# Kernel optimization log

Hardware: AMD Instinct MI355X
Metric: run time of the kernel (lower is better)

The kernel has to match this reference:

```python
import jax, jax.numpy as jnp
import numpy as np

B, DIM, HEADS, H, W = 4, 192, 6, 256, 256
C = DIM // HEADS  # channels per head
DN = ('NCHW', 'OIHW', 'NCHW')


def conv2d(x, w, b, padding='VALID', groups=1):
    y = jax.lax.conv_general_dilated(x, w, (1, 1), padding,
                                     dimension_numbers=DN,
                                     feature_group_count=groups)
    return y + b[None, :, None, None]


def setup_inputs() -> dict:
    key = jax.random.key(0)
    ks = jax.random.split(key, 8)
    s = 0.02
    return {
        'x': jax.random.normal(ks[0], (B, DIM, H, W), jnp.float32),
        'qkv_w': jax.random.normal(ks[1], (3 * DIM, DIM, 1, 1), jnp.float32) * s,
        'qkv_b': jnp.zeros((3 * DIM,), jnp.float32),
        'dw_w': jax.random.normal(ks[2], (3 * DIM, 1, 3, 3), jnp.float32) * s,
        'dw_b': jnp.zeros((3 * DIM,), jnp.float32),
        'proj_w': jax.random.normal(ks[3], (DIM, DIM, 1, 1), jnp.float32) * s,
        'proj_b': jnp.zeros((DIM,), jnp.float32),
        'temperature': jnp.ones((HEADS, 1, 1, 1), jnp.float32),
    }


def reference(x, qkv_w, qkv_b, dw_w, dw_b, proj_w, proj_b, temperature):
    # qkv projection: 1x1 conv then 3x3 depthwise conv
    qkv = conv2d(x, qkv_w, qkv_b)
    qkv = conv2d(qkv, dw_w, dw_b, padding='SAME', groups=3 * DIM)
    q, k, v = jnp.split(qkv, 3, axis=1)  # each (B, DIM, H, W)

    def heads(t):
        return t.reshape(B, HEADS, C, H, W)
    q, k, v = heads(q), heads(k), heads(v)

    # L2-normalize along W (matches F.normalize eps=1e-12)
    eps = 1e-12
    q = q / jnp.maximum(jnp.linalg.norm(q, axis=-1, keepdims=True), eps)
    k = k / jnp.maximum(jnp.linalg.norm(k, axis=-1, keepdims=True), eps)

    # per-channel HxH attention, contraction over W; temperature broadcasts over head
    attn = jnp.einsum('bncxw,bncyw->bncxy', q, k) * temperature  # (B,HEADS,C,H,H)
    attn = jax.nn.softmax(attn, axis=-1)
    out = jnp.einsum('bncxy,bncyw->bncxw', attn, v)  # (B,HEADS,C,H,W)

    out = out.reshape(B, DIM, H, W)
    return conv2d(out, proj_w, proj_b)
```

## Files before the change

### kernel.cpp

```cpp
#include <hip/hip_runtime.h>
#include <hip/hip_bf16.h>
#include <math.h>


#define HW 65536
#define IMW 256

typedef short bf16x8 __attribute__((ext_vector_type(8)));
typedef float f32x4  __attribute__((ext_vector_type(4)));

__device__ __forceinline__ float bf2f(ushort u) {
    return __uint_as_float((uint)u << 16);
}
__device__ __forceinline__ ushort f2bf(float f) {
    uint i = __float_as_uint(f);
    return (ushort)((i + 0x7FFFu + ((i >> 16) & 1u)) >> 16);
}

__device__ __forceinline__ void gload16(const ushort* g, ushort* l) {
    __builtin_amdgcn_global_load_lds(
        (const __attribute__((address_space(1))) void*)g,
        (__attribute__((address_space(3))) void*)l,
        16, 0, 0);
}

__global__ __launch_bounds__(256) void cvt_f32_bf16(const float* __restrict__ s,
                                                    ushort* __restrict__ d, int n)
{
    int i = blockIdx.x * 256 + threadIdx.x;
    if (i < n) d[i] = f2bf(s[i]);
}

__global__ __launch_bounds__(256) void cvt_transpose_f32(const float* __restrict__ src,
                                                         ushort* __restrict__ dst,
                                                         int R, int C,
                                                         long ssS, long ssD)
{
    __shared__ ushort Ls[64][72];
    int t = threadIdx.x;
    long z = blockIdx.z;
    src += z * ssS; dst += z * ssD;
    int c0 = blockIdx.x * 64, r0 = blockIdx.y * 64;
    {
        int r = t >> 2, cs = t & 3;
        const float* gp = src + (size_t)(r0 + r) * C + c0 + cs * 16;
        ushort tmp[16];
        #pragma unroll
        for (int q = 0; q < 4; ++q) {
            float4 v = *(const float4*)(gp + q * 4);
            tmp[q*4+0] = f2bf(v.x); tmp[q*4+1] = f2bf(v.y);
            tmp[q*4+2] = f2bf(v.z); tmp[q*4+3] = f2bf(v.w);
        }
        *(uint4*)&Ls[r][cs * 16]     = *(uint4*)&tmp[0];
        *(uint4*)&Ls[r][cs * 16 + 8] = *(uint4*)&tmp[8];
    }
    __syncthreads();
    {
        int cc = t & 63, seg = t >> 6;
        ushort tmp[16];
        #pragma unroll
        for (int j = 0; j < 16; ++j) tmp[j] = Ls[seg * 16 + j][cc];
        ushort* op = dst + (size_t)(c0 + cc) * R + r0 + seg * 16;
        *(uint4*)(op)     = *(uint4*)&tmp[0];
        *(uint4*)(op + 8) = *(uint4*)&tmp[8];
    }
}

__global__ __launch_bounds__(256) void transpose_bf16(const ushort* __restrict__ src,
                                                      ushort* __restrict__ dst,
                                                      int R, int C,
                                                      long ssS, long ssD)
{
    __shared__ ushort Ls[64][72];
    int t = threadIdx.x;
    long z = blockIdx.z;
    src += z * ssS; dst += z * ssD;
    int c0 = blockIdx.x * 64, r0 = blockIdx.y * 64;
    {
        int r = t >> 2, cs = t & 3;
        const ushort* gp = src + (size_t)(r0 + r) * C + c0 + cs * 16;
        *(uint4*)&Ls[r][cs * 16]     = *(const uint4*)(gp);
        *(uint4*)&Ls[r][cs * 16 + 8] = *(const uint4*)(gp + 8);
    }
    __syncthreads();
    {
        int cc = t & 63, seg = t >> 6;
        ushort tmp[16];
        #pragma unroll
        for (int j = 0; j < 16; ++j) tmp[j] = Ls[seg * 16 + j][cc];
        ushort* op = dst + (size_t)(c0 + cc) * R + r0 + seg * 16;
        *(uint4*)(op)     = *(uint4*)&tmp[0];
        *(uint4*)(op + 8) = *(uint4*)&tmp[8];
    }
}

__global__ __launch_bounds__(256) void transpose_v(const ushort* __restrict__ post,
                                                   ushort* __restrict__ vt)
{
    __shared__ ushort Ls[64][72];
    int t = threadIdx.x;
    int s = blockIdx.z;
    int b = s / 192, r = s - b * 192;
    const ushort* src = post + ((size_t)b * 576 + 384 + r) * HW;
    ushort*       dst = vt + (size_t)s * HW;
    int c0 = blockIdx.x * 64, r0 = blockIdx.y * 64;
    {
        int rr = t >> 2, cs = t & 3;
        const ushort* gp = src + (size_t)(r0 + rr) * IMW + c0 + cs * 16;
        *(uint4*)&Ls[rr][cs * 16]     = *(const uint4*)(gp);
        *(uint4*)&Ls[rr][cs * 16 + 8] = *(const uint4*)(gp + 8);
    }
    __syncthreads();
    {
        int cc = t & 63, seg = t >> 6;
        ushort tmp[16];
        #pragma unroll
        for (int j = 0; j < 16; ++j) tmp[j] = Ls[seg * 16 + j][cc];
        ushort* op = dst + (size_t)(c0 + cc) * IMW + r0 + seg * 16;
        *(uint4*)(op)     = *(uint4*)&tmp[0];
        *(uint4*)(op + 8) = *(uint4*)&tmp[8];
    }
}

__global__ __launch_bounds__(256) void gemm_mfma(const ushort* __restrict__ A, int lda, long sliceA,
                                                 const ushort* __restrict__ B, int ldb, long sliceB,
                                                 void* __restrict__ Dp, int ldd, long sliceD,
                                                 const float* __restrict__ bias,
                                                 int K, int outF32, int NM, int NN)
{
    int lin = blockIdx.x;
    int r8 = lin & 7, kk_ = lin >> 3;
    int m = kk_ % NM, fg = kk_ / NM;
    int g = fg * 8 + r8;
    int nt_ = g % NN;
    long z = g / NN;
    int m0 = m * 64;
    int n0 = nt_ * 256;

    __shared__ ushort Ws[2][64][32];
    __shared__ ushort Xs[2][256][32];
    int t = threadIdx.x, wv = t >> 6, lane = t & 63;
    int fr = lane & 15, sg = lane >> 4;
    A += z * sliceA; B += z * sliceB;

    int rl   = wv * 16 + (lane >> 2);
    int chnk = (lane & 3) ^ ((lane >> 3) & 3);
    const ushort* srcA  = A + (size_t)(m0 + rl) * lda + chnk * 8;
    const ushort* srcB0 = B + (size_t)(n0 +       rl) * ldb + chnk * 8;
    const ushort* srcB1 = B + (size_t)(n0 +  64 + rl) * ldb + chnk * 8;
    const ushort* srcB2 = B + (size_t)(n0 + 128 + rl) * ldb + chnk * 8;
    const ushort* srcB3 = B + (size_t)(n0 + 192 + rl) * ldb + chnk * 8;

    int sp = sg ^ ((fr >> 1) & 3);

    f32x4 acc[4][4];
    #pragma unroll
    for (int i = 0; i < 4; ++i)
        #pragma unroll
        for (int j = 0; j < 4; ++j) acc[i][j] = (f32x4){0.f, 0.f, 0.f, 0.f};

    gload16(srcA,  &Ws[0][wv * 16][0]);
    gload16(srcB0, &Xs[0][      wv * 16][0]);
    gload16(srcB1, &Xs[0][ 64 + wv * 16][0]);
    gload16(srcB2, &Xs[0][128 + wv * 16][0]);
    gload16(srcB3, &Xs[0][192 + wv * 16][0]);
    __syncthreads();

    int nkit = K >> 5;
    for (int kit = 0; kit < nkit; ++kit) {
        int cur = kit & 1;
        if (kit + 1 < nkit) {
            int kn = (kit + 1) * 32;
            gload16(srcA  + kn, &Ws[cur ^ 1][wv * 16][0]);
            gload16(srcB0 + kn, &Xs[cur ^ 1][      wv * 16][0]);
            gload16(srcB1 + kn, &Xs[cur ^ 1][ 64 + wv * 16][0]);
            gload16(srcB2 + kn, &Xs[cur ^ 1][128 + wv * 16][0]);
            gload16(srcB3 + kn, &Xs[cur ^ 1][192 + wv * 16][0]);
        }
        bf16x8 a[4];
        #pragma unroll
        for (int i = 0; i < 4; ++i)
            a[i] = *(const bf16x8*)&Ws[cur][i * 16 + fr][sp * 8];
        #pragma unroll
        for (int j = 0; j < 4; ++j) {
            bf16x8 b = *(const bf16x8*)&Xs[cur][wv * 64 + j * 16 + fr][sp * 8];
            #pragma unroll
            for (int i = 0; i < 4; ++i)
                acc[i][j] = __builtin_amdgcn_mfma_f32_16x16x32_bf16(a[i], b, acc[i][j], 0, 0, 0);
        }
        __syncthreads();
    }

    int nw0 = n0 + wv * 64;
    int rbase = sg * 4;
    if (outF32) {
        float* D = (float*)Dp + z * sliceD;
        #pragma unroll
        for (int i = 0; i < 4; ++i) {
            #pragma unroll
            for (int r_ = 0; r_ < 4; ++r_) {
                int mrow = m0 + i * 16 + rbase + r_;
                float bv = bias ? bias[mrow] : 0.f;
                #pragma unroll
                for (int j = 0; j < 4; ++j)
                    D[(size_t)mrow * ldd + nw0 + j * 16 + fr] = acc[i][j][r_] + bv;
            }
        }
    } else {
        ushort* D = (ushort*)Dp + z * sliceD;
        #pragma unroll
        for (int i = 0; i < 4; ++i) {
            #pragma unroll
            for (int r_ = 0; r_ < 4; ++r_) {
                int mrow = m0 + i * 16 + rbase + r_;
                float bv = bias ? bias[mrow] : 0.f;
                #pragma unroll
                for (int j = 0; j < 4; ++j)
                    D[(size_t)mrow * ldd + nw0 + j * 16 + fr] = f2bf(acc[i][j][r_] + bv);
            }
        }
    }
}

__global__ __launch_bounds__(256) void attn_fused(const ushort* __restrict__ post,
                                                  const ushort* __restrict__ vt,
                                                  const float* __restrict__ temp,
                                                  ushort* __restrict__ O)
{
    __shared__ ushort Ws[64][32];
    __shared__ ushort Xs[256][32];
    __shared__ ushort Ps[64][264];
    int t = threadIdx.x, wv = t >> 6, lane = t & 63;
    int fr = lane & 15, sg = lane >> 4;
    int lin = blockIdx.x;
    int r8 = lin & 7, k_ = lin >> 3;
    int mtile = k_ & 3, fg = k_ >> 2;
    int s = fg * 8 + r8;
    int b = s / 192, ch = s - b * 192;
    const ushort* Aq = post + ((size_t)b * 576 + ch) * HW;
    const ushort* Bk = Aq + (size_t)192 * HW;
    const ushort* Vt = vt + (size_t)s * HW;
    int m0 = mtile * 64;

    int rl   = wv * 16 + (lane >> 2);
    int chnk = (lane & 3) ^ ((lane >> 3) & 3);
    int sp   = sg ^ ((fr >> 1) & 3);
    const ushort* srcQ  = Aq + (size_t)(m0 + rl) * IMW + chnk * 8;
    const ushort* srcK0 = Bk + (size_t)(      rl) * IMW + chnk * 8;
    const ushort* srcK1 = Bk + (size_t)( 64 + rl) * IMW + chnk * 8;
    const ushort* srcK2 = Bk + (size_t)(128 + rl) * IMW + chnk * 8;
    const ushort* srcK3 = Bk + (size_t)(192 + rl) * IMW + chnk * 8;
    const ushort* srcV0 = Vt + (size_t)(      rl) * IMW + chnk * 8;
    const ushort* srcV1 = Vt + (size_t)( 64 + rl) * IMW + chnk * 8;
    const ushort* srcV2 = Vt + (size_t)(128 + rl) * IMW + chnk * 8;
    const ushort* srcV3 = Vt + (size_t)(192 + rl) * IMW + chnk * 8;

    f32x4 acc[16];
    #pragma unroll
    for (int i = 0; i < 16; ++i) acc[i] = (f32x4){0.f, 0.f, 0.f, 0.f};

    for (int k0 = 0; k0 < 256; k0 += 32) {
        gload16(srcQ  + k0, &Ws[wv * 16][0]);
        gload16(srcK0 + k0, &Xs[      wv * 16][0]);
        gload16(srcK1 + k0, &Xs[ 64 + wv * 16][0]);
        gload16(srcK2 + k0, &Xs[128 + wv * 16][0]);
        gload16(srcK3 + k0, &Xs[192 + wv * 16][0]);
        __syncthreads();
        bf16x8 a = *(const bf16x8*)&Ws[wv * 16 + fr][sp * 8];
        #pragma unroll
        for (int nt = 0; nt < 16; ++nt) {
            bf16x8 bfrag = *(const bf16x8*)&Xs[nt * 16 + fr][sp * 8];
            acc[nt] = __builtin_amdgcn_mfma_f32_16x16x32_bf16(a, bfrag, acc[nt], 0, 0, 0);
        }
        __syncthreads();
    }

    float tv = temp[ch >> 5];
    #pragma unroll
    for (int r_ = 0; r_ < 4; ++r_) {
        float v[16];
        float mx = -3.4e38f;
        #pragma unroll
        for (int nt = 0; nt < 16; ++nt) { v[nt] = acc[nt][r_] * tv; mx = fmaxf(mx, v[nt]); }
        #pragma unroll
        for (int sh = 1; sh < 16; sh <<= 1) mx = fmaxf(mx, __shfl_xor(mx, sh, 64));
        float sum = 0.f;
        #pragma unroll
        for (int nt = 0; nt < 16; ++nt) { v[nt] = __expf(v[nt] - mx); sum += v[nt]; }
        #pragma unroll
        for (int sh = 1; sh < 16; sh <<= 1) sum += __shfl_xor(sum, sh, 64);
        float inv = 1.f / sum;
        int ml = wv * 16 + sg * 4 + r_;
        #pragma unroll
        for (int nt = 0; nt < 16; ++nt)
            Ps[ml][fr + nt * 16] = f2bf(v[nt] * inv);
    }

    f32x4 acc2[16];
    #pragma unroll
    for (int i = 0; i < 16; ++i) acc2[i] = (f32x4){0.f, 0.f, 0.f, 0.f};

    for (int y0 = 0; y0 < 256; y0 += 32) {
        gload16(srcV0 + y0, &Xs[      wv * 16][0]);
        gload16(srcV1 + y0, &Xs[ 64 + wv * 16][0]);
        gload16(srcV2 + y0, &Xs[128 + wv * 16][0]);
        gload16(srcV3 + y0, &Xs[192 + wv * 16][0]);
        __syncthreads();
        bf16x8 a = *(const bf16x8*)&Ps[wv * 16 + fr][y0 + sg * 8];
        #pragma unroll
        for (int nt = 0; nt < 16; ++nt) {
            bf16x8 bfrag = *(const bf16x8*)&Xs[nt * 16 + fr][sp * 8];
            acc2[nt] = __builtin_amdgcn_mfma_f32_16x16x32_bf16(a, bfrag, acc2[nt], 0, 0, 0);
        }
        __syncthreads();
    }

    ushort* Op = O + (size_t)s * HW;
    int mrow = m0 + wv * 16 + sg * 4;
    #pragma unroll
    for (int r_ = 0; r_ < 4; ++r_) {
        #pragma unroll
        for (int nt = 0; nt < 16; ++nt)
            Op[(size_t)(mrow + r_) * IMW + fr + nt * 16] = f2bf(acc2[nt][r_]);
    }
}

__global__ __launch_bounds__(256) void dw3x3_l2norm(const ushort* __restrict__ in,
                                                    const float* __restrict__ w,
                                                    const float* __restrict__ bias,
                                                    ushort* __restrict__ out)
{
    int t = threadIdx.x;
    int lane = t & 63, wv = t >> 6;
    int ch = blockIdx.y;
    int r0 = blockIdx.x * 16 + wv * 4;
    const ushort* img  = in  + ((size_t)blockIdx.z * 576 + ch) * HW;
    ushort*       outp = out + ((size_t)blockIdx.z * 576 + ch) * HW;
    int px = lane * 4;

    float rv[6][4], lv[6], rx[6];
    #pragma unroll
    for (int i = 0; i < 6; ++i) {
        int rr = r0 - 1 + i;
        if ((unsigned)rr <= 255u) {
            ushort4 cv = *(const ushort4*)&img[(size_t)rr * IMW + px];
            rv[i][0] = bf2f(cv.x); rv[i][1] = bf2f(cv.y);
            rv[i][2] = bf2f(cv.z); rv[i][3] = bf2f(cv.w);
        } else {
            rv[i][0] = rv[i][1] = rv[i][2] = rv[i][3] = 0.f;
        }
        float l = __shfl_up(rv[i][3], 1, 64);
        lv[i] = (lane == 0) ? 0.f : l;
        float r = __shfl_down(rv[i][0], 1, 64);
        rx[i] = (lane == 63) ? 0.f : r;
    }

    const float* wch = w + ch * 9;
    float bv = bias[ch];
    bool do_norm = (ch < 384);

    #pragma unroll
    for (int j = 0; j < 4; ++j) {
        float a0 = bv, a1 = bv, a2 = bv, a3 = bv;
        #pragma unroll
        for (int dy = 0; dy < 3; ++dy) {
            int i = j + dy;
            float w0 = wch[dy * 3], w1 = wch[dy * 3 + 1], w2 = wch[dy * 3 + 2];
            a0 += lv[i]    * w0 + rv[i][0] * w1 + rv[i][1] * w2;
            a1 += rv[i][0] * w0 + rv[i][1] * w1 + rv[i][2] * w2;
            a2 += rv[i][1] * w0 + rv[i][2] * w1 + rv[i][3] * w2;
            a3 += rv[i][2] * w0 + rv[i][3] * w1 + rx[i]    * w2;
        }
        if (do_norm) {
            float ss = a0 * a0 + a1 * a1 + a2 * a2 + a3 * a3;
            #pragma unroll
            for (int m = 1; m < 64; m <<= 1) ss += __shfl_xor(ss, m, 64);
            float inv = 1.0f / fmaxf(sqrtf(ss), 1e-12f);
            a0 *= inv; a1 *= inv; a2 *= inv; a3 *= inv;
        }
        ushort4 o;
        o.x = f2bf(a0); o.y = f2bf(a1); o.z = f2bf(a2); o.w = f2bf(a3);
        *(ushort4*)&outp[(size_t)(r0 + j) * IMW + px] = o;
    }
}

extern "C" void kernel_launch(void* const* d_in, const int* in_sizes, int n_in,
                              void* d_out, int out_size, void* d_ws, size_t ws_size,
                              hipStream_t stream)
{
    const float* x      = (const float*)d_in[0];
    const float* qkv_w  = (const float*)d_in[1];
    const float* qkv_b  = (const float*)d_in[2];
    const float* dw_w   = (const float*)d_in[3];
    const float* dw_b   = (const float*)d_in[4];
    const float* proj_w = (const float*)d_in[5];
    const float* proj_b = (const float*)d_in[6];
    const float* temp   = (const float*)d_in[7];
    float* out = (float*)d_out;

    const size_t off_wq   = 0;
    const size_t off_wp   = 110592;
    const size_t off_pre  = 262144;
    const size_t off_post = off_pre + (size_t)4 * 576 * HW;
    const size_t off_xt   = off_post + (size_t)4 * 576 * HW;
    const size_t total_us = off_xt + (size_t)4 * 192 * HW;
    if (ws_size < total_us * sizeof(ushort)) return;

    ushort* wsb  = (ushort*)d_ws;
    ushort* wq   = wsb + off_wq;
    ushort* wp   = wsb + off_wp;
    ushort* pre  = wsb + off_pre;
    ushort* post = wsb + off_post;
    ushort* xt   = wsb + off_xt;
    ushort* Obuf = pre;
    ushort* Otb  = pre + (size_t)4 * 192 * HW;

    const long SL = (long)192 * HW;

    cvt_f32_bf16<<<dim3(432), 256, 0, stream>>>(qkv_w, wq, 110592);
    cvt_f32_bf16<<<dim3(144), 256, 0, stream>>>(proj_w, wp, 36864);

    cvt_transpose_f32<<<dim3(1024, 3, 4), 256, 0, stream>>>(x, xt, 192, HW, SL, SL);
    gemm_mfma<<<dim3(9 * 256 * 4), 256, 0, stream>>>(wq, 192, 0, xt, 192, SL,
                                                     pre, HW, (long)576 * HW,
                                                     qkv_b, 192, 0, 9, 256);
    dw3x3_l2norm<<<dim3(16, 576, 4), 256, 0, stream>>>(pre, dw_w, dw_b, post);
    transpose_v<<<dim3(4, 4, 768), 256, 0, stream>>>(post, xt);
    attn_fused<<<dim3(4 * 768), 256, 0, stream>>>(post, xt, temp, Obuf);
    transpose_bf16<<<dim3(1024, 3, 4), 256, 0, stream>>>(Obuf, Otb, 192, HW, SL, SL);
    gemm_mfma<<<dim3(3 * 256 * 4), 256, 0, stream>>>(wp, 192, 0, Otb, 192, SL,
                                                     out, HW, SL,
                                                     proj_b, 192, 1, 3, 256);
}
```

Measured before the change: 687.7 us.

## Double-buffer LDS loads in fused attention and enlarge depthwise row tiles

Both GEMM phases of the fused attention kernel now use two LDS buffers, so the global-to-LDS load of the next K chunk is issued before computing the current one, and one barrier per iteration is dropped. The first V tile is prefetched while the softmax runs. Separately, the depthwise 3x3 plus L2-norm kernel now has each wave process 8 rows instead of 4, which cuts the halo reloads by half and launches half as many blocks. LDS use for the K/V staging doubles and the depthwise kernel holds more registers, which may reduce occupancy.

Result: slower. 718.5 us (+4.5%).

```diff
diff --git a/kernel.cpp b/kernel.cpp
--- a/kernel.cpp
+++ b/kernel.cpp
@@ -227,8 +227,8 @@
                                                   const float* __restrict__ temp,
                                                   ushort* __restrict__ O)
 {
-    __shared__ ushort Ws[64][32];
-    __shared__ ushort Xs[256][32];
+    __shared__ ushort Ws[2][64][32];
+    __shared__ ushort Xs[2][256][32];
     __shared__ ushort Ps[64][264];
     int t = threadIdx.x, wv = t >> 6, lane = t & 63;
     int fr = lane & 15, sg = lane >> 4;
@@ -259,21 +259,36 @@
     #pragma unroll
     for (int i = 0; i < 16; ++i) acc[i] = (f32x4){0.f, 0.f, 0.f, 0.f};
 
-    for (int k0 = 0; k0 < 256; k0 += 32) {
-        gload16(srcQ  + k0, &Ws[wv * 16][0]);
-        gload16(srcK0 + k0, &Xs[      wv * 16][0]);
-        gload16(srcK1 + k0, &Xs[ 64 + wv * 16][0]);
-        gload16(srcK2 + k0, &Xs[128 + wv * 16][0]);
-        gload16(srcK3 + k0, &Xs[192 + wv * 16][0]);
+    gload16(srcQ,  &Ws[0][wv * 16][0]);
+    gload16(srcK0, &Xs[0][      wv * 16][0]);
+    gload16(srcK1, &Xs[0][ 64 + wv * 16][0]);
+    gload16(srcK2, &Xs[0][128 + wv * 16][0]);
+    gload16(srcK3, &Xs[0][192 + wv * 16][0]);
+    __syncthreads();
+
+    for (int kit = 0; kit < 8; ++kit) {
+        int cur = kit & 1;
+        if (kit < 7) {
+            int kn = (kit + 1) * 32;
+            gload16(srcQ  + kn, &Ws[cur ^ 1][wv * 16][0]);
+            gload16(srcK0 + kn, &Xs[cur ^ 1][      wv * 16][0]);
+            gload16(srcK1 + kn, &Xs[cur ^ 1][ 64 + wv * 16][0]);
+            gload16(srcK2 + kn, &Xs[cur ^ 1][128 + wv * 16][0]);
+            gload16(srcK3 + kn, &Xs[cur ^ 1][192 + wv * 16][0]);
+        }
+        bf16x8 a = *(const bf16x8*)&Ws[cur][wv * 16 + fr][sp * 8];
+        #pragma unroll
+        for (int nt = 0; nt < 16; ++nt) {
+            bf16x8 bfrag = *(const bf16x8*)&Xs[cur][nt * 16 + fr][sp * 8];
+            acc[nt] = __builtin_amdgcn_mfma_f32_16x16x32_bf16(a, bfrag, acc[nt], 0, 0, 0);
+        }
         __syncthreads();
-        bf16x8 a = *(const bf16x8*)&Ws[wv * 16 + fr][sp * 8];
-        #pragma unroll
-        for (int nt = 0; nt < 16; ++nt) {
-            bf16x8 bfrag = *(const bf16x8*)&Xs[nt * 16 + fr][sp * 8];
-            acc[nt] = __builtin_amdgcn_mfma_f32_16x16x32_bf16(a, bfrag, acc[nt], 0, 0, 0);
-        }
-        __syncthreads();
-    }
+    }
+
+    gload16(srcV0, &Xs[0][      wv * 16][0]);
+    gload16(srcV1, &Xs[0][ 64 + wv * 16][0]);
+    gload16(srcV2, &Xs[0][128 + wv * 16][0]);
+    gload16(srcV3, &Xs[0][192 + wv * 16][0]);
 
     float tv = temp[ch >> 5];
     #pragma unroll
@@ -295,21 +310,25 @@
         for (int nt = 0; nt < 16; ++nt)
             Ps[ml][fr + nt * 16] = f2bf(v[nt] * inv);
     }
+    __syncthreads();
 
     f32x4 acc2[16];
     #pragma unroll
     for (int i = 0; i < 16; ++i) acc2[i] = (f32x4){0.f, 0.f, 0.f, 0.f};
 
-    for (int y0 = 0; y0 < 256; y0 += 32) {
-        gload16(srcV0 + y0, &Xs[      wv * 16][0]);
-        gload16(srcV1 + y0, &Xs[ 64 + wv * 16][0]);
-        gload16(srcV2 + y0, &Xs[128 + wv * 16][0]);
-        gload16(srcV3 + y0, &Xs[192 + wv * 16][0]);
-        __syncthreads();
-        bf16x8 a = *(const bf16x8*)&Ps[wv * 16 + fr][y0 + sg * 8];
+    for (int y = 0; y < 8; ++y) {
+        int cur = y & 1;
+        if (y < 7) {
+            int yn = (y + 1) * 32;
+            gload16(srcV0 + yn, &Xs[cur ^ 1][      wv * 16][0]);
+            gload16(srcV1 + yn, &Xs[cur ^ 1][ 64 + wv * 16][0]);
+            gload16(srcV2 + yn, &Xs[cur ^ 1][128 + wv * 16][0]);
+            gload16(srcV3 + yn, &Xs[cur ^ 1][192 + wv * 16][0]);
+        }
+        bf16x8 a = *(const bf16x8*)&Ps[wv * 16 + fr][y * 32 + sg * 8];
         #pragma unroll
         for (int nt = 0; nt < 16; ++nt) {
-            bf16x8 bfrag = *(const bf16x8*)&Xs[nt * 16 + fr][sp * 8];
+            bf16x8 bfrag = *(const bf16x8*)&Xs[cur][nt * 16 + fr][sp * 8];
             acc2[nt] = __builtin_amdgcn_mfma_f32_16x16x32_bf16(a, bfrag, acc2[nt], 0, 0, 0);
         }
         __syncthreads();
@@ -333,14 +352,14 @@
     int t = threadIdx.x;
     int lane = t & 63, wv = t >> 6;
     int ch = blockIdx.y;
-    int r0 = blockIdx.x * 16 + wv * 4;
+    int r0 = blockIdx.x * 32 + wv * 8;
     const ushort* img  = in  + ((size_t)blockIdx.z * 576 + ch) * HW;
     ushort*       outp = out + ((size_t)blockIdx.z * 576 + ch) * HW;
     int px = lane * 4;
 
-    float rv[6][4], lv[6], rx[6];
-    #pragma unroll
-    for (int i = 0; i < 6; ++i) {
+    float rv[10][4], lv[10], rx[10];
+    #pragma unroll
+    for (int i = 0; i < 10; ++i) {
         int rr = r0 - 1 + i;
         if ((unsigned)rr <= 255u) {
             ushort4 cv = *(const ushort4*)&img[(size_t)rr * IMW + px];
@@ -360,7 +379,7 @@
     bool do_norm = (ch < 384);
 
     #pragma unroll
-    for (int j = 0; j < 4; ++j) {
+    for (int j = 0; j < 8; ++j) {
         float a0 = bv, a1 = bv, a2 = bv, a3 = bv;
         #pragma unroll
         for (int dy = 0; dy < 3; ++dy) {
@@ -424,7 +443,7 @@
     gemm_mfma<<<dim3(9 * 256 * 4), 256, 0, stream>>>(wq, 192, 0, xt, 192, SL,
                                                      pre, HW, (long)576 * HW,
                                                      qkv_b, 192, 0, 9, 256);
-    dw3x3_l2norm<<<dim3(16, 576, 4), 256, 0, stream>>>(pre, dw_w, dw_b, post);
+    dw3x3_l2norm<<<dim3(8, 576, 4), 256, 0, stream>>>(pre, dw_w, dw_b, post);
     transpose_v<<<dim3(4, 4, 768), 256, 0, stream>>>(post, xt);
     attn_fused<<<dim3(4 * 768), 256, 0, stream>>>(post, xt, temp, Obuf);
     transpose_bf16<<<dim3(1024, 3, 4), 256, 0, stream>>>(Obuf, Otb, 192, HW, SL, SL);
```
